# Kernel tuning notes

Measured on AMD Instinct MI355X. Metric: run time of the kernel, lower is better.

## Reference

```python
import jax, jax.numpy as jnp
import numpy as np

L, B, D = 50, 1024, 512      # memory slots, batch, d_model
H, DK = 4, 512               # heads, per-head dim (d_k = d_model in this module)
HOP = 3


def setup_inputs() -> dict:
    key = jax.random.key(0)
    ks = jax.random.split(key, 16)
    s = lambda i, shape: jax.random.normal(ks[i], shape, jnp.float32) * 0.02
    return dict(
        momery=jax.random.normal(ks[0], (L, B, D), jnp.float32),
        hid=jax.random.normal(ks[1], (B, D), jnp.float32),
        text_polarity=jax.random.normal(ks[2], (B,), jnp.float32),
        attribute_polarity=jax.random.normal(ks[3], (B,), jnp.float32),
        w=jnp.array(0.5, jnp.float32),
        p_w1=s(4, (D, D)), p_b1=jnp.zeros((D,), jnp.float32),
        p_w2=s(5, (D, D)), p_b2=jnp.zeros((D,), jnp.float32),
        wq=s(6, (D, H * DK)), bq=jnp.zeros((H * DK,), jnp.float32),
        wk=s(7, (D, H * DK)), bk=jnp.zeros((H * DK,), jnp.float32),
        wv=s(8, (D, H * DK)), bv=jnp.zeros((H * DK,), jnp.float32),
        wo=s(9, (H * DK, D)), bo=jnp.zeros((D,), jnp.float32),
    )


def reference(momery, hid, text_polarity, attribute_polarity, w,
              p_w1, p_b1, p_w2, p_b2, wq, bq, wk, bk, wv, bv, wo, bo):
    # k, v depend only on hid (attinkv = hid every hop/slot) -> hoist out of hop loop
    k = (hid @ wk + bk).reshape(B, H, DK)   # [B,H,DK]
    v = (hid @ wv + bv).reshape(B, H, DK)   # [B,H,DK]
    inv_sqrt_dk = jnp.float32(1.0 / np.sqrt(DK))
    for _ in range(HOP):
        # projection MLP over all slots at once (replaces per-slot loop)
        mid = jax.nn.relu(momery @ p_w1 + p_b1) @ p_w2 + p_b2          # [L,B,D]
        q = (mid @ wq + bq).reshape(L, B, H, DK)                        # [L,B,H,DK]
        # single key per query (nk=1): scores [L,B,H,1], softmax -> ones
        scores = (jnp.einsum('lbhd,bhd->lbh', q, k) * inv_sqrt_dk)[..., None]
        att = jax.nn.softmax(scores, axis=-1)                           # [L,B,H,1]
        out = att * v                                                   # [L,B,H,DK]
        temp = out.reshape(L, B, H * DK) @ wo + bo                      # [L,B,D]
        momery = momery + w * temp
    return momery
```

## Files before the change

### kernel.cpp

```cpp
#include <hip/hip_runtime.h>

#define B_SZ 1024
#define D_SZ 512
#define LDSP 68

__device__ __forceinline__ float4 f4add(float4 a, float4 b) {
    return make_float4(a.x + b.x, a.y + b.y, a.z + b.z, a.w + b.w);
}

__global__ __launch_bounds__(256) void gemmA(const float* __restrict__ wv,
                                             const float* __restrict__ wo,
                                             const float* __restrict__ bv,
                                             const float* __restrict__ bo,
                                             float* __restrict__ Wp,
                                             float* __restrict__ b2p) {
    __shared__ float As[32 * LDSP];
    __shared__ float Bs[32 * LDSP];

    const int tid  = threadIdx.x;
    const int col0 = blockIdx.x * 64;
    const int row0 = blockIdx.y * 64;
    const int z    = blockIdx.z;
    const int k0   = z * 512;
    constexpr int K = 2048, N = 512, NT = 16;

    const int aR = tid >> 3;
    const int aK = (tid & 7) << 2;
    const int bK = tid >> 4;
    const int bC = (tid & 15) << 2;
    const int ty = (tid >> 4) << 2;
    const int tx = (tid & 15) << 2;

    const float* pa0 = wv + (size_t)(row0 + aR) * K + k0 + aK;
    const float* pa1 = pa0 + (size_t)32 * K;
    const float* pb0 = wo + (size_t)(k0 + bK) * N + col0 + bC;
    const float* pb1 = pb0 + (size_t)16 * N;

    float4 a0 = *(const float4*)pa0;
    float4 a1 = *(const float4*)pa1;
    float4 b0 = *(const float4*)pb0;
    float4 b1 = *(const float4*)pb1;

    float acc[4][4] = {};

    for (int t = 0; t < NT; ++t) {
        __syncthreads();
        As[(aK + 0) * LDSP + aR] = a0.x;
        As[(aK + 1) * LDSP + aR] = a0.y;
        As[(aK + 2) * LDSP + aR] = a0.z;
        As[(aK + 3) * LDSP + aR] = a0.w;
        As[(aK + 0) * LDSP + aR + 32] = a1.x;
        As[(aK + 1) * LDSP + aR + 32] = a1.y;
        As[(aK + 2) * LDSP + aR + 32] = a1.z;
        As[(aK + 3) * LDSP + aR + 32] = a1.w;
        *(float4*)(Bs + bK * LDSP + bC) = b0;
        *(float4*)(Bs + (bK + 16) * LDSP + bC) = b1;
        if (t + 1 < NT) {
            pa0 += 32; pa1 += 32;
            pb0 += (size_t)32 * N; pb1 += (size_t)32 * N;
            a0 = *(const float4*)pa0;
            a1 = *(const float4*)pa1;
            b0 = *(const float4*)pb0;
            b1 = *(const float4*)pb1;
        }
        __syncthreads();
#pragma unroll
        for (int kk = 0; kk < 32; ++kk) {
            float4 av = *(const float4*)(As + kk * LDSP + ty);
            float4 bv4 = *(const float4*)(Bs + kk * LDSP + tx);
            float ar[4] = {av.x, av.y, av.z, av.w};
            float br[4] = {bv4.x, bv4.y, bv4.z, bv4.w};
#pragma unroll
            for (int i = 0; i < 4; ++i)
#pragma unroll
                for (int j = 0; j < 4; ++j) acc[i][j] += ar[i] * br[j];
        }
    }

    float* C = Wp + (size_t)z * 262144;
    const int r0 = row0 + ty, c0 = col0 + tx;
#pragma unroll
    for (int i = 0; i < 4; ++i)
        *(float4*)(C + (size_t)(r0 + i) * N + c0) =
            make_float4(acc[i][0], acc[i][1], acc[i][2], acc[i][3]);

    if (z == 0) {
        int bid = blockIdx.y * 8 + blockIdx.x;
        int g = bid * 256 + tid;
        int o = g & 511;
        int r = g >> 9;
        float s = (r == 0) ? bo[o] : 0.f;
        int j0 = r * 64;
#pragma unroll 8
        for (int j = j0; j < j0 + 64; ++j) s += bv[j] * wo[j * 512 + o];
        b2p[r * 512 + o] = s;
    }
}

__global__ __launch_bounds__(256) void gemmB(const float* __restrict__ hid,
                                             const float* __restrict__ Wp,
                                             const float* __restrict__ b2p,
                                             float* __restrict__ t0,
                                             float* __restrict__ t1) {
    __shared__ float As[32 * LDSP];
    __shared__ float Bs[32 * LDSP];

    const int tid  = threadIdx.x;
    const int col0 = blockIdx.x * 64;
    const int row0 = blockIdx.y * 64;
    const int z    = blockIdx.z;
    const int k0   = z * 256;
    constexpr int K = 512, N = 512, NT = 8;

    const int aR = tid >> 3;
    const int aK = (tid & 7) << 2;
    const int bK = tid >> 4;
    const int bC = (tid & 15) << 2;
    const int ty = (tid >> 4) << 2;
    const int tx = (tid & 15) << 2;

    const float* pa0 = hid + (size_t)(row0 + aR) * K + k0 + aK;
    const float* pa1 = pa0 + (size_t)32 * K;
    const float* pb0 = Wp + (size_t)(k0 + bK) * N + col0 + bC;
    const float* pb1 = pb0 + (size_t)16 * N;

    float4 a0 = *(const float4*)pa0;
    float4 a1 = *(const float4*)pa1;
    float4 vb0[4], vb1[4];
#pragma unroll
    for (int p = 0; p < 4; ++p) {
        vb0[p] = *(const float4*)(pb0 + (size_t)p * 262144);
        vb1[p] = *(const float4*)(pb1 + (size_t)p * 262144);
    }

    float acc[4][4] = {};

    for (int t = 0; t < NT; ++t) {
        float4 sb0 = f4add(f4add(vb0[0], vb0[1]), f4add(vb0[2], vb0[3]));
        float4 sb1 = f4add(f4add(vb1[0], vb1[1]), f4add(vb1[2], vb1[3]));
        __syncthreads();
        As[(aK + 0) * LDSP + aR] = a0.x;
        As[(aK + 1) * LDSP + aR] = a0.y;
        As[(aK + 2) * LDSP + aR] = a0.z;
        As[(aK + 3) * LDSP + aR] = a0.w;
        As[(aK + 0) * LDSP + aR + 32] = a1.x;
        As[(aK + 1) * LDSP + aR + 32] = a1.y;
        As[(aK + 2) * LDSP + aR + 32] = a1.z;
        As[(aK + 3) * LDSP + aR + 32] = a1.w;
        *(float4*)(Bs + bK * LDSP + bC) = sb0;
        *(float4*)(Bs + (bK + 16) * LDSP + bC) = sb1;
        if (t + 1 < NT) {
            pa0 += 32; pa1 += 32;
            pb0 += (size_t)32 * N; pb1 += (size_t)32 * N;
            a0 = *(const float4*)pa0;
            a1 = *(const float4*)pa1;
#pragma unroll
            for (int p = 0; p < 4; ++p) {
                vb0[p] = *(const float4*)(pb0 + (size_t)p * 262144);
                vb1[p] = *(const float4*)(pb1 + (size_t)p * 262144);
            }
        }
        __syncthreads();
#pragma unroll
        for (int kk = 0; kk < 32; ++kk) {
            float4 av = *(const float4*)(As + kk * LDSP + ty);
            float4 bv4 = *(const float4*)(Bs + kk * LDSP + tx);
            float ar[4] = {av.x, av.y, av.z, av.w};
            float br[4] = {bv4.x, bv4.y, bv4.z, bv4.w};
#pragma unroll
            for (int i = 0; i < 4; ++i)
#pragma unroll
                for (int j = 0; j < 4; ++j) acc[i][j] += ar[i] * br[j];
        }
    }

    __syncthreads();
    if (z == 0 && tid < 64) {
        float s = 0.f;
#pragma unroll 8
        for (int r = 0; r < 32; ++r) s += b2p[r * 512 + col0 + tid];
        Bs[tid] = s;
    }
    __syncthreads();
    float4 bb = make_float4(0, 0, 0, 0);
    if (z == 0) bb = *(const float4*)(Bs + tx);

    float* C = z ? t1 : t0;
    const int r0 = row0 + ty, c0 = col0 + tx;
#pragma unroll
    for (int i = 0; i < 4; ++i)
        *(float4*)(C + (size_t)(r0 + i) * N + c0) =
            make_float4(acc[i][0] + bb.x, acc[i][1] + bb.y,
                        acc[i][2] + bb.z, acc[i][3] + bb.w);
}

__global__ __launch_bounds__(256) void bcast_add_kernel(const float* __restrict__ mem,
                                                        const float* __restrict__ t0,
                                                        const float* __restrict__ t1,
                                                        const float* __restrict__ wp,
                                                        float* __restrict__ out) {
    int idx = blockIdx.x * 256 + threadIdx.x;
    const float4 mv = ((const float4*)mem)[idx];
    int bd = idx & ((B_SZ * D_SZ / 4) - 1);
    const float4 a = ((const float4*)t0)[bd];
    const float4 b = ((const float4*)t1)[bd];
    float s = 3.0f * wp[0];
    float4 o;
    o.x = mv.x + s * (a.x + b.x);
    o.y = mv.y + s * (a.y + b.y);
    o.z = mv.z + s * (a.z + b.z);
    o.w = mv.w + s * (a.w + b.w);
    ((float4*)out)[idx] = o;
}

extern "C" void kernel_launch(void* const* d_in, const int* in_sizes, int n_in,
                              void* d_out, int out_size, void* d_ws, size_t ws_size,
                              hipStream_t stream) {
    const float* momery = (const float*)d_in[0];
    const float* hid    = (const float*)d_in[1];
    const float* w      = (const float*)d_in[4];
    const float* wv     = (const float*)d_in[13];
    const float* bv     = (const float*)d_in[14];
    const float* wo     = (const float*)d_in[15];
    const float* bo     = (const float*)d_in[16];
    float* out = (float*)d_out;

    float* Wp  = (float*)d_ws;
    float* b2p = Wp + 4 * 262144;
    float* t0  = b2p + 16384;
    float* t1  = t0 + 524288;

    gemmA<<<dim3(8, 8, 4), 256, 0, stream>>>(wv, wo, bv, bo, Wp, b2p);

    gemmB<<<dim3(8, 16, 2), 256, 0, stream>>>(hid, Wp, b2p, t0, t1);

    bcast_add_kernel<<<25600, 256, 0, stream>>>(momery, t0, t1, w, out);
}
```

Measured before the change: 257.4 us.

## Use bf16 MFMA instructions for both GEMMs instead of fp32 LDS tiling

Replaces the LDS-tiled fp32 FMA inner loops in gemmA and gemmB with direct register loads converted to bf16 and fed to 16x16x32 bf16 MFMA instructions, removing shared memory staging and block barriers from the main loop. Each wave computes a 32x32 tile from four MFMA accumulators. Inputs are rounded to bf16, which reduces precision of the folded weight and hidden projections. B-operand loads are now scalar strided column reads instead of float4 rows, which may be less coalesced.

```diff
diff --git a/kernel.cpp b/kernel.cpp
--- a/kernel.cpp
+++ b/kernel.cpp
@@ -1,11 +1,15 @@
 #include <hip/hip_runtime.h>
+#include <hip/hip_bf16.h>
 
 #define B_SZ 1024
 #define D_SZ 512
-#define LDSP 68
-
-__device__ __forceinline__ float4 f4add(float4 a, float4 b) {
-    return make_float4(a.x + b.x, a.y + b.y, a.z + b.z, a.w + b.w);
+
+typedef short short8 __attribute__((ext_vector_type(8)));
+typedef float f4 __attribute__((ext_vector_type(4)));
+
+__device__ __forceinline__ short f2bfs(float f) {
+    __hip_bfloat16 h = __float2bfloat16(f);
+    return __builtin_bit_cast(short, h);
 }
 
 __global__ __launch_bounds__(256) void gemmA(const float* __restrict__ wv,
@@ -14,75 +18,73 @@
                                              const float* __restrict__ bo,
                                              float* __restrict__ Wp,
                                              float* __restrict__ b2p) {
-    __shared__ float As[32 * LDSP];
-    __shared__ float Bs[32 * LDSP];
-
+    constexpr int K = 2048, N = 512, NT = 16;
     const int tid  = threadIdx.x;
     const int col0 = blockIdx.x * 64;
     const int row0 = blockIdx.y * 64;
     const int z    = blockIdx.z;
     const int k0   = z * 512;
-    constexpr int K = 2048, N = 512, NT = 16;
-
-    const int aR = tid >> 3;
-    const int aK = (tid & 7) << 2;
-    const int bK = tid >> 4;
-    const int bC = (tid & 15) << 2;
-    const int ty = (tid >> 4) << 2;
-    const int tx = (tid & 15) << 2;
-
-    const float* pa0 = wv + (size_t)(row0 + aR) * K + k0 + aK;
-    const float* pa1 = pa0 + (size_t)32 * K;
-    const float* pb0 = wo + (size_t)(k0 + bK) * N + col0 + bC;
-    const float* pb1 = pb0 + (size_t)16 * N;
-
-    float4 a0 = *(const float4*)pa0;
-    float4 a1 = *(const float4*)pa1;
-    float4 b0 = *(const float4*)pb0;
-    float4 b1 = *(const float4*)pb1;
-
-    float acc[4][4] = {};
+
+    const int lane = tid & 63;
+    const int wave = tid >> 6;
+    const int mq = wave >> 1, nq = wave & 1;
+    const int ln = lane & 15, q = lane >> 4;
+
+    const int rowA0 = row0 + mq * 32 + ln;
+    const int rowA1 = rowA0 + 16;
+    const int colB0 = col0 + nq * 32 + ln;
+    const int colB1 = colB0 + 16;
+
+    const float* pa0 = wv + (size_t)rowA0 * K + k0 + q * 8;
+    const float* pa1 = wv + (size_t)rowA1 * K + k0 + q * 8;
+    const float* pb  = wo + (size_t)(k0 + q * 8) * N;
+
+    float4 a00 = *(const float4*)pa0, a01 = *(const float4*)(pa0 + 4);
+    float4 a10 = *(const float4*)pa1, a11 = *(const float4*)(pa1 + 4);
+    float b0r[8], b1r[8];
+#pragma unroll
+    for (int j = 0; j < 8; ++j) {
+        b0r[j] = pb[(size_t)j * N + colB0];
+        b1r[j] = pb[(size_t)j * N + colB1];
+    }
+
+    f4 acc00 = {0,0,0,0}, acc01 = {0,0,0,0}, acc10 = {0,0,0,0}, acc11 = {0,0,0,0};
 
     for (int t = 0; t < NT; ++t) {
-        __syncthreads();
-        As[(aK + 0) * LDSP + aR] = a0.x;
-        As[(aK + 1) * LDSP + aR] = a0.y;
-        As[(aK + 2) * LDSP + aR] = a0.z;
-        As[(aK + 3) * LDSP + aR] = a0.w;
-        As[(aK + 0) * LDSP + aR + 32] = a1.x;
-        As[(aK + 1) * LDSP + aR + 32] = a1.y;
-        As[(aK + 2) * LDSP + aR + 32] = a1.z;
-        As[(aK + 3) * LDSP + aR + 32] = a1.w;
-        *(float4*)(Bs + bK * LDSP + bC) = b0;
-        *(float4*)(Bs + (bK + 16) * LDSP + bC) = b1;
+        short8 af0, af1, bf0, bf1;
+        af0[0]=f2bfs(a00.x); af0[1]=f2bfs(a00.y); af0[2]=f2bfs(a00.z); af0[3]=f2bfs(a00.w);
+        af0[4]=f2bfs(a01.x); af0[5]=f2bfs(a01.y); af0[6]=f2bfs(a01.z); af0[7]=f2bfs(a01.w);
+        af1[0]=f2bfs(a10.x); af1[1]=f2bfs(a10.y); af1[2]=f2bfs(a10.z); af1[3]=f2bfs(a10.w);
+        af1[4]=f2bfs(a11.x); af1[5]=f2bfs(a11.y); af1[6]=f2bfs(a11.z); af1[7]=f2bfs(a11.w);
+#pragma unroll
+        for (int j = 0; j < 8; ++j) { bf0[j] = f2bfs(b0r[j]); bf1[j] = f2bfs(b1r[j]); }
+
         if (t + 1 < NT) {
-            pa0 += 32; pa1 += 32;
-            pb0 += (size_t)32 * N; pb1 += (size_t)32 * N;
-            a0 = *(const float4*)pa0;
-            a1 = *(const float4*)pa1;
-            b0 = *(const float4*)pb0;
-            b1 = *(const float4*)pb1;
+            pa0 += 32; pa1 += 32; pb += (size_t)32 * N;
+            a00 = *(const float4*)pa0; a01 = *(const float4*)(pa0 + 4);
+            a10 = *(const float4*)pa1; a11 = *(const float4*)(pa1 + 4);
+#pragma unroll
+            for (int j = 0; j < 8; ++j) {
+                b0r[j] = pb[(size_t)j * N + colB0];
+                b1r[j] = pb[(size_t)j * N + colB1];
+            }
         }
-        __syncthreads();
-#pragma unroll
-        for (int kk = 0; kk < 32; ++kk) {
-            float4 av = *(const float4*)(As + kk * LDSP + ty);
-            float4 bv4 = *(const float4*)(Bs + kk * LDSP + tx);
-            float ar[4] = {av.x, av.y, av.z, av.w};
-            float br[4] = {bv4.x, bv4.y, bv4.z, bv4.w};
-#pragma unroll
-            for (int i = 0; i < 4; ++i)
-#pragma unroll
-                for (int j = 0; j < 4; ++j) acc[i][j] += ar[i] * br[j];
-        }
+        acc00 = __builtin_amdgcn_mfma_f32_16x16x32_bf16(af0, bf0, acc00, 0, 0, 0);
+        acc01 = __builtin_amdgcn_mfma_f32_16x16x32_bf16(af0, bf1, acc01, 0, 0, 0);
+        acc10 = __builtin_amdgcn_mfma_f32_16x16x32_bf16(af1, bf0, acc10, 0, 0, 0);
+        acc11 = __builtin_amdgcn_mfma_f32_16x16x32_bf16(af1, bf1, acc11, 0, 0, 0);
     }
 
     float* C = Wp + (size_t)z * 262144;
-    const int r0 = row0 + ty, c0 = col0 + tx;
-#pragma unroll
-    for (int i = 0; i < 4; ++i)
-        *(float4*)(C + (size_t)(r0 + i) * N + c0) =
-            make_float4(acc[i][0], acc[i][1], acc[i][2], acc[i][3]);
+    const int r0 = row0 + mq * 32 + q * 4;
+    const int c0 = col0 + nq * 32 + ln;
+#pragma unroll
+    for (int r = 0; r < 4; ++r) {
+        C[(size_t)(r0 + r) * N + c0]           = acc00[r];
+        C[(size_t)(r0 + r) * N + c0 + 16]      = acc01[r];
+        C[(size_t)(r0 + 16 + r) * N + c0]      = acc10[r];
+        C[(size_t)(r0 + 16 + r) * N + c0 + 16] = acc11[r];
+    }
 
     if (z == 0) {
         int bid = blockIdx.y * 8 + blockIdx.x;
@@ -102,96 +104,91 @@
                                              const float* __restrict__ b2p,
                                              float* __restrict__ t0,
                                              float* __restrict__ t1) {
-    __shared__ float As[32 * LDSP];
-    __shared__ float Bs[32 * LDSP];
+    constexpr int K = 512, N = 512, NT = 8;
+    __shared__ float biasS[64];
 
     const int tid  = threadIdx.x;
     const int col0 = blockIdx.x * 64;
     const int row0 = blockIdx.y * 64;
     const int z    = blockIdx.z;
     const int k0   = z * 256;
-    constexpr int K = 512, N = 512, NT = 8;
-
-    const int aR = tid >> 3;
-    const int aK = (tid & 7) << 2;
-    const int bK = tid >> 4;
-    const int bC = (tid & 15) << 2;
-    const int ty = (tid >> 4) << 2;
-    const int tx = (tid & 15) << 2;
-
-    const float* pa0 = hid + (size_t)(row0 + aR) * K + k0 + aK;
-    const float* pa1 = pa0 + (size_t)32 * K;
-    const float* pb0 = Wp + (size_t)(k0 + bK) * N + col0 + bC;
-    const float* pb1 = pb0 + (size_t)16 * N;
-
-    float4 a0 = *(const float4*)pa0;
-    float4 a1 = *(const float4*)pa1;
-    float4 vb0[4], vb1[4];
-#pragma unroll
-    for (int p = 0; p < 4; ++p) {
-        vb0[p] = *(const float4*)(pb0 + (size_t)p * 262144);
-        vb1[p] = *(const float4*)(pb1 + (size_t)p * 262144);
-    }
-
-    float acc[4][4] = {};
+
+    const int lane = tid & 63;
+    const int wave = tid >> 6;
+    const int mq = wave >> 1, nq = wave & 1;
+    const int ln = lane & 15, q = lane >> 4;
+
+    const int rowA0 = row0 + mq * 32 + ln;
+    const int rowA1 = rowA0 + 16;
+    const int colB0 = col0 + nq * 32 + ln;
+    const int colB1 = colB0 + 16;
+
+    const float* pa0 = hid + (size_t)rowA0 * K + k0 + q * 8;
+    const float* pa1 = hid + (size_t)rowA1 * K + k0 + q * 8;
+    const float* pb  = Wp + (size_t)(k0 + q * 8) * N;
+
+    float4 a00 = *(const float4*)pa0, a01 = *(const float4*)(pa0 + 4);
+    float4 a10 = *(const float4*)pa1, a11 = *(const float4*)(pa1 + 4);
+    float b0r[8], b1r[8];
+#pragma unroll
+    for (int j = 0; j < 8; ++j) {
+        size_t off = (size_t)j * N;
+        b0r[j] = pb[off + colB0]           + pb[off + colB0 + 262144]
+               + pb[off + colB0 + 524288]  + pb[off + colB0 + 786432];
+        b1r[j] = pb[off + colB1]           + pb[off + colB1 + 262144]
+               + pb[off + colB1 + 524288]  + pb[off + colB1 + 786432];
+    }
+
+    f4 acc00 = {0,0,0,0}, acc01 = {0,0,0,0}, acc10 = {0,0,0,0}, acc11 = {0,0,0,0};
 
     for (int t = 0; t < NT; ++t) {
-        float4 sb0 = f4add(f4add(vb0[0], vb0[1]), f4add(vb0[2], vb0[3]));
-        float4 sb1 = f4add(f4add(vb1[0], vb1[1]), f4add(vb1[2], vb1[3]));
-        __syncthreads();
-        As[(aK + 0) * LDSP + aR] = a0.x;
-        As[(aK + 1) * LDSP + aR] = a0.y;
-        As[(aK + 2) * LDSP + aR] = a0.z;
-        As[(aK + 3) * LDSP + aR] = a0.w;
-        As[(aK + 0) * LDSP + aR + 32] = a1.x;
-        As[(aK + 1) * LDSP + aR + 32] = a1.y;
-        As[(aK + 2) * LDSP + aR + 32] = a1.z;
-        As[(aK + 3) * LDSP + aR + 32] = a1.w;
-        *(float4*)(Bs + bK * LDSP + bC) = sb0;
-        *(float4*)(Bs + (bK + 16) * LDSP + bC) = sb1;
+        short8 af0, af1, bf0, bf1;
+        af0[0]=f2bfs(a00.x); af0[1]=f2bfs(a00.y); af0[2]=f2bfs(a00.z); af0[3]=f2bfs(a00.w);
+        af0[4]=f2bfs(a01.x); af0[5]=f2bfs(a01.y); af0[6]=f2bfs(a01.z); af0[7]=f2bfs(a01.w);
+        af1[0]=f2bfs(a10.x); af1[1]=f2bfs(a10.y); af1[2]=f2bfs(a10.z); af1[3]=f2bfs(a10.w);
+        af1[4]=f2bfs(a11.x); af1[5]=f2bfs(a11.y); af1[6]=f2bfs(a11.z); af1[7]=f2bfs(a11.w);
+#pragma unroll
+        for (int j = 0; j < 8; ++j) { bf0[j] = f2bfs(b0r[j]); bf1[j] = f2bfs(b1r[j]); }
+
         if (t + 1 < NT) {
-            pa0 += 32; pa1 += 32;
-            pb0 += (size_t)32 * N; pb1 += (size_t)32 * N;
-            a0 = *(const float4*)pa0;
-            a1 = *(const float4*)pa1;
-#pragma unroll
-            for (int p = 0; p < 4; ++p) {
-                vb0[p] = *(const float4*)(pb0 + (size_t)p * 262144);
-                vb1[p] = *(const float4*)(pb1 + (size_t)p * 262144);
+            pa0 += 32; pa1 += 32; pb += (size_t)32 * N;
+            a00 = *(const float4*)pa0; a01 = *(const float4*)(pa0 + 4);
+            a10 = *(const float4*)pa1; a11 = *(const float4*)(pa1 + 4);
+#pragma unroll
+            for (int j = 0; j < 8; ++j) {
+                size_t off = (size_t)j * N;
+                b0r[j] = pb[off + colB0]           + pb[off + colB0 + 262144]
+                       + pb[off + colB0 + 524288]  + pb[off + colB0 + 786432];
+                b1r[j] = pb[off + colB1]           + pb[off + colB1 + 262144]
+                       + pb[off + colB1 + 524288]  + pb[off + colB1 + 786432];
             }
         }
-        __syncthreads();
-#pragma unroll
-        for (int kk = 0; kk < 32; ++kk) {
-            float4 av = *(const float4*)(As + kk * LDSP + ty);
-            float4 bv4 = *(const float4*)(Bs + kk * LDSP + tx);
-            float ar[4] = {av.x, av.y, av.z, av.w};
-            float br[4] = {bv4.x, bv4.y, bv4.z, bv4.w};
-#pragma unroll
-            for (int i = 0; i < 4; ++i)
-#pragma unroll
-                for (int j = 0; j < 4; ++j) acc[i][j] += ar[i] * br[j];
-        }
-    }
-
-    __syncthreads();
+        acc00 = __builtin_amdgcn_mfma_f32_16x16x32_bf16(af0, bf0, acc00, 0, 0, 0);
+        acc01 = __builtin_amdgcn_mfma_f32_16x16x32_bf16(af0, bf1, acc01, 0, 0, 0);
+        acc10 = __builtin_amdgcn_mfma_f32_16x16x32_bf16(af1, bf0, acc10, 0, 0, 0);
+        acc11 = __builtin_amdgcn_mfma_f32_16x16x32_bf16(af1, bf1, acc11, 0, 0, 0);
+    }
+
     if (z == 0 && tid < 64) {
         float s = 0.f;
 #pragma unroll 8
         for (int r = 0; r < 32; ++r) s += b2p[r * 512 + col0 + tid];
-        Bs[tid] = s;
+        biasS[tid] = s;
     }
     __syncthreads();
-    float4 bb = make_float4(0, 0, 0, 0);
-    if (z == 0) bb = *(const float4*)(Bs + tx);
+    float bj0 = 0.f, bj1 = 0.f;
+    if (z == 0) { bj0 = biasS[nq * 32 + ln]; bj1 = biasS[nq * 32 + 16 + ln]; }
 
     float* C = z ? t1 : t0;
-    const int r0 = row0 + ty, c0 = col0 + tx;
-#pragma unroll
-    for (int i = 0; i < 4; ++i)
-        *(float4*)(C + (size_t)(r0 + i) * N + c0) =
-            make_float4(acc[i][0] + bb.x, acc[i][1] + bb.y,
-                        acc[i][2] + bb.z, acc[i][3] + bb.w);
+    const int r0 = row0 + mq * 32 + q * 4;
+    const int c0 = col0 + nq * 32 + ln;
+#pragma unroll
+    for (int r = 0; r < 4; ++r) {
+        C[(size_t)(r0 + r) * N + c0]           = acc00[r] + bj0;
+        C[(size_t)(r0 + r) * N + c0 + 16]      = acc01[r] + bj1;
+        C[(size_t)(r0 + 16 + r) * N + c0]      = acc10[r] + bj0;
+        C[(size_t)(r0 + 16 + r) * N + c0 + 16] = acc11[r] + bj1;
+    }
 }
 
 __global__ __launch_bounds__(256) void bcast_add_kernel(const float* __restrict__ mem,
```

New measurement: 252.0 us. -2.1%, faster.
